# Performance work log

Hardware: AMD Instinct MI355X
Metric: run time of the kernel (lower is better)

The kernel has to match this reference:

```python
import jax, jax.numpy as jnp
import numpy as np

B, D, C = 8192, 2048, 1000
EPS32 = float(np.finfo(np.float32).eps)      # torch clamp_probs uses finfo.eps
LOG_2PI = float(np.log(2.0 * np.pi))
GAMMA = float(1.0 / np.exp(100.0))           # lerp at global_step=0 -> start_val = 1/exp(start_rho)


def setup_inputs() -> dict:
    key = jax.random.key(0)
    k = jax.random.split(key, 6)
    feature = jax.random.normal(k[0], (B, D), jnp.float32)
    target = jax.random.randint(k[1], (B,), 0, C)
    eps = jax.random.normal(k[2], (B, D), jnp.float32)
    # y_project: Linear(C, D) -> weight [D, C], bias [D]
    y_w = jax.random.normal(k[3], (D, C), jnp.float32) * 0.02
    y_b = jnp.zeros((D,), jnp.float32)
    # cls_project: Linear(D, C) -> weight [C, D], bias [C]
    # small weights + positive bias keep Categorical probs positive (torch would
    # clamp negatives to eps; we replicate the clamp but avoid degenerate NaNs)
    cls_w = jax.random.normal(k[4], (C, D), jnp.float32) * 0.001
    cls_b = jnp.ones((C,), jnp.float32) * 5.0
    return dict(feature=feature, y_w=y_w, y_b=y_b, cls_w=cls_w, cls_b=cls_b,
                eps=eps, target=target)


def reference(feature, y_w, y_b, cls_w, cls_b, eps, target):
    # z = m.sample() : identity-covariance MVN sample, detached (torch .sample())
    z = jax.lax.stop_gradient(feature + eps)                      # [B, D]

    # y_emb = y_project(one_hot(target)) == gather of weight columns + bias
    y_emb = jnp.take(y_w, target, axis=1).T + y_b                 # [B, D]

    # Categorical(probs=cls_project(z)): normalize, clamp, log
    probs_raw = z @ cls_w.T + cls_b                               # [B, C]
    p = probs_raw / jnp.sum(probs_raw, axis=-1, keepdims=True)
    logits = jnp.log(jnp.clip(p, EPS32, 1.0 - EPS32))             # [B, C]

    # identity-covariance MVN log_prob in closed form
    const = 0.5 * D * LOG_2PI
    h1 = 0.5 * jnp.sum((z - feature) ** 2, axis=-1) + const       # -m.log_prob(z)
    h2 = 0.5 * jnp.sum((z - y_emb) ** 2, axis=-1) + const         # -y_emb_d.log_prob(z)
    h3 = -jnp.take_along_axis(logits, target[:, None], axis=1)[:, 0]

    rex = h2 - h1
    loss = jnp.mean(jnp.float32(GAMMA) * rex + h3)
    return logits, loss
```

## Files before the change

kernel.cpp:

```cpp
#include <hip/hip_runtime.h>
#include <hip/hip_bf16.h>

#define B_ROWS 8192
#define D_DIM  2048
#define C_DIM  1000
#define C_PAD  1024

#define EPS32   1.1920928955078125e-07f
#define GAMMA_F 3.7200759760208361e-44f

typedef __attribute__((ext_vector_type(8))) short short8;
typedef __attribute__((ext_vector_type(4))) float f32x4;

#define GLOAD_LDS16(gptr, lptr) \
  __builtin_amdgcn_global_load_lds((const __attribute__((address_space(1))) void*)(gptr), \
                                   (__attribute__((address_space(3))) void*)(lptr), 16, 0, 0)

__device__ inline unsigned short f2bf(float x) {
  union { __hip_bfloat16 b; unsigned short u; } cv;
  cv.b = __float2bfloat16(x);
  return cv.u;
}

__device__ inline float wave_red(float v) {
#pragma unroll
  for (int off = 32; off > 0; off >>= 1) v += __shfl_down(v, off, 64);
  return v;
}

__global__ __launch_bounds__(256) void prep_clsw(const float* __restrict__ cls_w,
                                                 __hip_bfloat16* __restrict__ out) {
  int j = (blockIdx.x * 256 + threadIdx.x) * 8;
  int row = j >> 11;
  int col = j & 2047;
  union { unsigned short u[8]; uint4 v; } pk;
  if (row < C_DIM) {
    const float* src = cls_w + (size_t)row * D_DIM + col;
#pragma unroll
    for (int i = 0; i < 8; ++i) pk.u[i] = f2bf(src[i]);
  } else {
#pragma unroll
    for (int i = 0; i < 8; ++i) pk.u[i] = 0;
  }
  *(uint4*)((unsigned short*)out + j) = pk.v;
}

__global__ __launch_bounds__(256) void prep_ywt(const float* __restrict__ y_w,
                                                const float* __restrict__ y_b,
                                                float* __restrict__ out) {
  int idx = blockIdx.x * 256 + threadIdx.x;
  int t = idx >> 11;
  int d = idx & 2047;
  out[idx] = y_w[(size_t)d * C_DIM + t] + y_b[d];
}

__global__ __launch_bounds__(256) void fuse_z(const float* __restrict__ feature,
                                              const float* __restrict__ eps,
                                              const float* __restrict__ ywtb,
                                              const int* __restrict__ target,
                                              __hip_bfloat16* __restrict__ z_bf,
                                              float* __restrict__ rex) {
  int b = blockIdx.x;
  int tid = threadIdx.x;
  int t = target[b];
  const float4* f4 = (const float4*)(feature + (size_t)b * D_DIM);
  const float4* e4 = (const float4*)(eps + (size_t)b * D_DIM);
  const float4* y4 = (const float4*)(ywtb + (size_t)t * D_DIM);
  uint2* zrow = (uint2*)((unsigned short*)z_bf + (size_t)b * D_DIM);

  float se = 0.f, sd = 0.f;
#pragma unroll
  for (int i = 0; i < 2; ++i) {
    int idx = tid + i * 256;
    float4 f = f4[idx];
    float4 e = e4[idx];
    float4 y = y4[idx];
    float z0 = f.x + e.x, z1 = f.y + e.y, z2 = f.z + e.z, z3 = f.w + e.w;
    union { unsigned short u[4]; uint2 v; } pz;
    pz.u[0] = f2bf(z0); pz.u[1] = f2bf(z1); pz.u[2] = f2bf(z2); pz.u[3] = f2bf(z3);
    zrow[idx] = pz.v;
    float a0 = z0 - f.x, a1 = z1 - f.y, a2 = z2 - f.z, a3 = z3 - f.w;
    se += a0 * a0 + a1 * a1 + a2 * a2 + a3 * a3;
    float g0 = z0 - y.x, g1 = z1 - y.y, g2 = z2 - y.z, g3 = z3 - y.w;
    sd += g0 * g0 + g1 * g1 + g2 * g2 + g3 * g3;
  }
  se = wave_red(se);
  sd = wave_red(sd);
  __shared__ float s1[4], s2[4];
  int lane = tid & 63, w = tid >> 6;
  if (lane == 0) { s1[w] = se; s2[w] = sd; }
  __syncthreads();
  if (tid == 0) {
    float S1 = s1[0] + s1[1] + s1[2] + s1[3];
    float S2 = s2[0] + s2[1] + s2[2] + s2[3];
    rex[b] = 0.5f * (S2 - S1);
  }
}

__global__ __launch_bounds__(256) void gemm_bt(const __hip_bfloat16* __restrict__ A,
                                               const __hip_bfloat16* __restrict__ Bt,
                                               const float* __restrict__ cls_b,
                                               float* __restrict__ out) {
  __shared__ __align__(16) __hip_bfloat16 sA[128 * 64];
  __shared__ __align__(16) __hip_bfloat16 sB[128 * 64];
  const int tid = threadIdx.x;
  const int m0 = blockIdx.x * 128;
  const int n0 = blockIdx.y * 128;
  const int w = tid >> 6, lane = tid & 63;
  const int wm = (w & 1) * 64, wn = (w >> 1) * 64;
  const int l15 = lane & 15, quad = lane >> 4;

  f32x4 acc[4][4] = {};

  for (int k0 = 0; k0 < D_DIM; k0 += 64) {
#pragma unroll
    for (int i = 0; i < 4; ++i) {
      int j = i * 256 + tid;
      int row = j >> 3, cc = j & 7;
      const __hip_bfloat16* srcA = A + (size_t)(m0 + row) * D_DIM + k0 + cc * 8;
      const __hip_bfloat16* srcB = Bt + (size_t)(n0 + row) * D_DIM + k0 + cc * 8;
      GLOAD_LDS16(srcA, &sA[j * 8]);
      GLOAD_LDS16(srcB, &sB[j * 8]);
    }
    __syncthreads();
#pragma unroll
    for (int kk = 0; kk < 64; kk += 32) {
      short8 af[4], bf[4];
#pragma unroll
      for (int i = 0; i < 4; ++i)
        af[i] = *(const short8*)&sA[(wm + i * 16 + l15) * 64 + kk + quad * 8];
#pragma unroll
      for (int jn = 0; jn < 4; ++jn)
        bf[jn] = *(const short8*)&sB[(wn + jn * 16 + l15) * 64 + kk + quad * 8];
#pragma unroll
      for (int i = 0; i < 4; ++i)
#pragma unroll
        for (int jn = 0; jn < 4; ++jn)
          acc[i][jn] = __builtin_amdgcn_mfma_f32_16x16x32_bf16(af[i], bf[jn], acc[i][jn], 0, 0, 0);
    }
    __syncthreads();
  }

#pragma unroll
  for (int i = 0; i < 4; ++i) {
    int row = m0 + wm + i * 16 + quad * 4;
#pragma unroll
    for (int jn = 0; jn < 4; ++jn) {
      int col = n0 + wn + jn * 16 + l15;
      if (col < C_DIM) {
        float bias = cls_b[col];
#pragma unroll
        for (int r = 0; r < 4; ++r)
          out[(size_t)(row + r) * C_DIM + col] = acc[i][jn][r] + bias;
      }
    }
  }
}

__global__ __launch_bounds__(256) void rownorm(float* __restrict__ out,
                                               const int* __restrict__ target,
                                               float* __restrict__ rowloss) {
  int b = blockIdx.x, tid = threadIdx.x;
  float* row = out + (size_t)b * C_DIM;
  float v[4];
  float s = 0.f;
#pragma unroll
  for (int i = 0; i < 4; ++i) {
    int c = tid + i * 256;
    v[i] = (c < C_DIM) ? row[c] : 0.f;
    s += v[i];
  }
  s = wave_red(s);
  __shared__ float ws_[4];
  __shared__ float h3s;
  int lane = tid & 63, w = tid >> 6;
  if (lane == 0) ws_[w] = s;
  __syncthreads();
  float total = ws_[0] + ws_[1] + ws_[2] + ws_[3];
  float inv = 1.0f / total;
  int t = target[b];
#pragma unroll
  for (int i = 0; i < 4; ++i) {
    int c = tid + i * 256;
    if (c < C_DIM) {
      float p = v[i] * inv;
      p = fminf(fmaxf(p, EPS32), 1.0f - EPS32);
      float lg = logf(p);
      row[c] = lg;
      if (c == t) h3s = -lg;
    }
  }
  __syncthreads();
  if (tid == 0) {
    float rx = rowloss[b];
    rowloss[b] = fmaf(GAMMA_F, rx, h3s);
  }
}

__global__ __launch_bounds__(256) void finalize(const float* __restrict__ rowloss,
                                                float* __restrict__ out_loss) {
  int tid = threadIdx.x;
  float s = 0.f;
  for (int i = tid; i < B_ROWS; i += 256) s += rowloss[i];
  s = wave_red(s);
  __shared__ float sm[4];
  if ((tid & 63) == 0) sm[tid >> 6] = s;
  __syncthreads();
  if (tid == 0) out_loss[0] = (sm[0] + sm[1] + sm[2] + sm[3]) * (1.0f / B_ROWS);
}

extern "C" void kernel_launch(void* const* d_in, const int* in_sizes, int n_in,
                              void* d_out, int out_size, void* d_ws, size_t ws_size,
                              hipStream_t stream) {
  const float* feature = (const float*)d_in[0];
  const float* y_w     = (const float*)d_in[1];
  const float* y_b     = (const float*)d_in[2];
  const float* cls_w   = (const float*)d_in[3];
  const float* cls_b   = (const float*)d_in[4];
  const float* eps     = (const float*)d_in[5];
  const int*   target  = (const int*)d_in[6];
  float* out = (float*)d_out;

  char* ws = (char*)d_ws;
  __hip_bfloat16* z_bf    = (__hip_bfloat16*)ws;
  __hip_bfloat16* clsw_bf = (__hip_bfloat16*)(ws + 33554432);
  float*          ywtb    = (float*)(ws + 33554432 + 4194304);
  float*          rex     = (float*)(ws + 33554432 + 4194304 + 8192000);

  prep_clsw<<<dim3(C_PAD * D_DIM / (256 * 8)), 256, 0, stream>>>(cls_w, clsw_bf);
  prep_ywt<<<dim3(C_DIM * D_DIM / 256), 256, 0, stream>>>(y_w, y_b, ywtb);
  fuse_z<<<dim3(B_ROWS), 256, 0, stream>>>(feature, eps, ywtb, target, z_bf, rex);
  gemm_bt<<<dim3(B_ROWS / 128, C_PAD / 128), 256, 0, stream>>>(z_bf, clsw_bf, cls_b, out);
  rownorm<<<dim3(B_ROWS), 256, 0, stream>>>(out, target, rex);
  finalize<<<dim3(1), 256, 0, stream>>>(rex, out + (size_t)B_ROWS * C_DIM);
}
```

Measured before the change: 266.0 us.

## Merge prep kernels with tiled transpose, shrink GEMM M-tile, use fast log

Merges the two weight-prep kernels into one launch. The y_w transpose now goes through a padded shared-memory tile, so both its reads and writes are coalesced instead of strided. The GEMM block tile drops from 128x128 to 64x128 with each wave owning a 64x32 slice, which doubles the grid (1024 blocks) to raise occupancy and wave count on the many-CU device, at the cost of less reuse of the B tile. rownorm swaps logf for __logf, trading a little precision for speed.

```diff
diff --git a/kernel.cpp b/kernel.cpp
--- a/kernel.cpp
+++ b/kernel.cpp
@@ -28,30 +28,46 @@
   return v;
 }
 
-__global__ __launch_bounds__(256) void prep_clsw(const float* __restrict__ cls_w,
-                                                 __hip_bfloat16* __restrict__ out) {
-  int j = (blockIdx.x * 256 + threadIdx.x) * 8;
-  int row = j >> 11;
-  int col = j & 2047;
-  union { unsigned short u[8]; uint4 v; } pk;
-  if (row < C_DIM) {
-    const float* src = cls_w + (size_t)row * D_DIM + col;
-#pragma unroll
-    for (int i = 0; i < 8; ++i) pk.u[i] = f2bf(src[i]);
+__global__ __launch_bounds__(256) void prep(const float* __restrict__ cls_w,
+                                            const float* __restrict__ y_w,
+                                            const float* __restrict__ y_b,
+                                            __hip_bfloat16* __restrict__ clsw_bf,
+                                            float* __restrict__ ywtb) {
+  __shared__ float tile[32][33];
+  int bid = blockIdx.x;
+  if (bid < 1024) {
+    int j = (bid * 256 + threadIdx.x) * 8;
+    int row = j >> 11;
+    int col = j & 2047;
+    union { unsigned short u[8]; uint4 v; } pk;
+    if (row < C_DIM) {
+      const float* src = cls_w + (size_t)row * D_DIM + col;
+#pragma unroll
+      for (int i = 0; i < 8; ++i) pk.u[i] = f2bf(src[i]);
+    } else {
+#pragma unroll
+      for (int i = 0; i < 8; ++i) pk.u[i] = 0;
+    }
+    *(uint4*)((unsigned short*)clsw_bf + j) = pk.v;
   } else {
-#pragma unroll
-    for (int i = 0; i < 8; ++i) pk.u[i] = 0;
-  }
-  *(uint4*)((unsigned short*)out + j) = pk.v;
-}
-
-__global__ __launch_bounds__(256) void prep_ywt(const float* __restrict__ y_w,
-                                                const float* __restrict__ y_b,
-                                                float* __restrict__ out) {
-  int idx = blockIdx.x * 256 + threadIdx.x;
-  int t = idx >> 11;
-  int d = idx & 2047;
-  out[idx] = y_w[(size_t)d * C_DIM + t] + y_b[d];
+    int b2 = bid - 1024;
+    int tb = b2 & 31, db = b2 >> 5;
+    int t0 = tb * 32, d0 = db * 32;
+    int tx = threadIdx.x & 31, ty = threadIdx.x >> 5;
+#pragma unroll
+    for (int r = 0; r < 4; ++r) {
+      int d = d0 + ty + r * 8;
+      int t = t0 + tx;
+      tile[ty + r * 8][tx] = (t < C_DIM) ? y_w[(size_t)d * C_DIM + t] : 0.f;
+    }
+    __syncthreads();
+#pragma unroll
+    for (int r = 0; r < 4; ++r) {
+      int t = t0 + ty + r * 8;
+      int d = d0 + tx;
+      if (t < C_DIM) ywtb[(size_t)t * D_DIM + d] = tile[tx][ty + r * 8] + y_b[d];
+    }
+  }
 }
 
 __global__ __launch_bounds__(256) void fuse_z(const float* __restrict__ feature,
@@ -101,51 +117,54 @@
                                                const __hip_bfloat16* __restrict__ Bt,
                                                const float* __restrict__ cls_b,
                                                float* __restrict__ out) {
-  __shared__ __align__(16) __hip_bfloat16 sA[128 * 64];
+  __shared__ __align__(16) __hip_bfloat16 sA[64 * 64];
   __shared__ __align__(16) __hip_bfloat16 sB[128 * 64];
   const int tid = threadIdx.x;
-  const int m0 = blockIdx.x * 128;
+  const int m0 = blockIdx.x * 64;
   const int n0 = blockIdx.y * 128;
   const int w = tid >> 6, lane = tid & 63;
-  const int wm = (w & 1) * 64, wn = (w >> 1) * 64;
+  const int wn = w * 32;
   const int l15 = lane & 15, quad = lane >> 4;
 
-  f32x4 acc[4][4] = {};
+  f32x4 acc[4][2] = {};
 
   for (int k0 = 0; k0 < D_DIM; k0 += 64) {
+#pragma unroll
+    for (int i = 0; i < 2; ++i) {
+      int j = i * 256 + tid;
+      int row = j >> 3, cc = j & 7;
+      GLOAD_LDS16(A + (size_t)(m0 + row) * D_DIM + k0 + cc * 8, &sA[j * 8]);
+    }
 #pragma unroll
     for (int i = 0; i < 4; ++i) {
       int j = i * 256 + tid;
       int row = j >> 3, cc = j & 7;
-      const __hip_bfloat16* srcA = A + (size_t)(m0 + row) * D_DIM + k0 + cc * 8;
-      const __hip_bfloat16* srcB = Bt + (size_t)(n0 + row) * D_DIM + k0 + cc * 8;
-      GLOAD_LDS16(srcA, &sA[j * 8]);
-      GLOAD_LDS16(srcB, &sB[j * 8]);
+      GLOAD_LDS16(Bt + (size_t)(n0 + row) * D_DIM + k0 + cc * 8, &sB[j * 8]);
     }
     __syncthreads();
 #pragma unroll
     for (int kk = 0; kk < 64; kk += 32) {
-      short8 af[4], bf[4];
+      short8 af[4], bfr[2];
 #pragma unroll
       for (int i = 0; i < 4; ++i)
-        af[i] = *(const short8*)&sA[(wm + i * 16 + l15) * 64 + kk + quad * 8];
-#pragma unroll
-      for (int jn = 0; jn < 4; ++jn)
-        bf[jn] = *(const short8*)&sB[(wn + jn * 16 + l15) * 64 + kk + quad * 8];
+        af[i] = *(const short8*)&sA[(i * 16 + l15) * 64 + kk + quad * 8];
+#pragma unroll
+      for (int jn = 0; jn < 2; ++jn)
+        bfr[jn] = *(const short8*)&sB[(wn + jn * 16 + l15) * 64 + kk + quad * 8];
 #pragma unroll
       for (int i = 0; i < 4; ++i)
 #pragma unroll
-        for (int jn = 0; jn < 4; ++jn)
-          acc[i][jn] = __builtin_amdgcn_mfma_f32_16x16x32_bf16(af[i], bf[jn], acc[i][jn], 0, 0, 0);
+        for (int jn = 0; jn < 2; ++jn)
+          acc[i][jn] = __builtin_amdgcn_mfma_f32_16x16x32_bf16(af[i], bfr[jn], acc[i][jn], 0, 0, 0);
     }
     __syncthreads();
   }
 
 #pragma unroll
   for (int i = 0; i < 4; ++i) {
-    int row = m0 + wm + i * 16 + quad * 4;
-#pragma unroll
-    for (int jn = 0; jn < 4; ++jn) {
+    int row = m0 + i * 16 + quad * 4;
+#pragma unroll
+    for (int jn = 0; jn < 2; ++jn) {
       int col = n0 + wn + jn * 16 + l15;
       if (col < C_DIM) {
         float bias = cls_b[col];
@@ -185,7 +204,7 @@
     if (c < C_DIM) {
       float p = v[i] * inv;
       p = fminf(fmaxf(p, EPS32), 1.0f - EPS32);
-      float lg = logf(p);
+      float lg = __logf(p);
       row[c] = lg;
       if (c == t) h3s = -lg;
     }
@@ -227,10 +246,9 @@
   float*          ywtb    = (float*)(ws + 33554432 + 4194304);
   float*          rex     = (float*)(ws + 33554432 + 4194304 + 8192000);
 
-  prep_clsw<<<dim3(C_PAD * D_DIM / (256 * 8)), 256, 0, stream>>>(cls_w, clsw_bf);
-  prep_ywt<<<dim3(C_DIM * D_DIM / 256), 256, 0, stream>>>(y_w, y_b, ywtb);
+  prep<<<dim3(1024 + 2048), 256, 0, stream>>>(cls_w, y_w, y_b, clsw_bf, ywtb);
   fuse_z<<<dim3(B_ROWS), 256, 0, stream>>>(feature, eps, ywtb, target, z_bf, rex);
-  gemm_bt<<<dim3(B_ROWS / 128, C_PAD / 128), 256, 0, stream>>>(z_bf, clsw_bf, cls_b, out);
+  gemm_bt<<<dim3(B_ROWS / 64, C_PAD / 128), 256, 0, stream>>>(z_bf, clsw_bf, cls_b, out);
   rownorm<<<dim3(B_ROWS), 256, 0, stream>>>(out, target, rex);
   finalize<<<dim3(1), 256, 0, stream>>>(rex, out + (size_t)B_ROWS * C_DIM);
 }
```

Result: no change. 262.1 us (-1.5%).
